# Kernel tuning notes

Measured on AMD Instinct MI355X. Metric: run time of the kernel, lower is better.

Reference implementation:

```python
import jax, jax.numpy as jnp
import numpy as np
from jax import lax

# module constants (from init_kwargs)
IN_CH = 128
OUT_CH = 128
CTX = 128
KS = 3
STRIDE = 1
PAD = 1
GROUPS = 1
ATT_GROUPS = 1
K = 4
TEMP = 30.0  # T_max, used as the fixed temperature at init


def setup_inputs() -> dict:
    key = jax.random.key(0)
    k1, k2, k3, k4, k5 = jax.random.split(key, 5)
    b, f, t = 16, 64, 256
    x = jax.random.normal(k1, (b, IN_CH, f, t), dtype=jnp.float32)
    g = jax.random.normal(k2, (1, b, CTX), dtype=jnp.float32)
    # Dense(k*att_groups) params (kaiming-normal kernel, zero bias)
    fan_in = CTX
    dense_kernel = jax.random.normal(k3, (CTX, K * ATT_GROUPS), dtype=jnp.float32) * np.sqrt(2.0 / fan_in)
    dense_bias = jnp.zeros((K * ATT_GROUPS,), dtype=jnp.float32)
    # kernel bank: (k, out, in//groups, ks, ks) -> swapaxes(1,2) -> flatten to (1, att_groups, k, -1)
    flat = OUT_CH * (IN_CH // GROUPS) * KS * KS // ATT_GROUPS
    weight = jax.random.normal(k4, (1, ATT_GROUPS, K, flat), dtype=jnp.float32) * np.sqrt(2.0 / flat)
    return {"x": x, "g": g, "dense_kernel": dense_kernel, "dense_bias": dense_bias, "weight": weight}


def reference(x, g, dense_kernel, dense_bias, weight):
    b, c, f, t = x.shape
    g_c = g[0].reshape(b, -1)                                  # [b, ctx]
    residuals = (g_c @ dense_kernel + dense_bias).reshape(b, ATT_GROUPS, 1, -1)  # [b, ag, 1, k]
    attention = jax.nn.softmax(residuals / TEMP, axis=-1)      # [b, ag, 1, k]
    # per-sample kernel aggregation: [b, ag, 1, k] @ [1, ag, k, D] -> [b, ag, 1, D]
    agg = (attention @ weight).swapaxes(1, 2)                  # [b, 1, ag, D]
    agg = agg.reshape(b * OUT_CH, IN_CH // GROUPS, KS, KS)
    # batch-as-groups grouped conv
    out = lax.conv_general_dilated(
        x.reshape(1, b * c, f, t), agg,
        window_strides=(STRIDE, STRIDE),
        padding=[(PAD, PAD), (PAD, PAD)],
        dimension_numbers=("NCHW", "OIHW", "NCHW"),
        feature_group_count=b * GROUPS,
    )
    return out.reshape(b, OUT_CH, out.shape[-2], out.shape[-1])
```

## Files before the change

### kernel.cpp

```cpp
#include <hip/hip_runtime.h>
#include <stdint.h>

#define NB 16
#define NC 128
#define NOC 128
#define NF 64
#define NT 256
#define NCTX 128
#define NTAPS 9
#define NFLAT 147456
#define TEMPR 30.0f

#define SXCOLS 130
#define SX_CHUNKS (4*SXCOLS)
#define SW_CHUNKS (3*4*NOC)

typedef float f32x4 __attribute__((ext_vector_type(4)));
typedef __bf16 bf16x8 __attribute__((ext_vector_type(8)));

__global__ void attn_kernel(const float* __restrict__ g,
                            const float* __restrict__ dk,
                            const float* __restrict__ bias,
                            float* __restrict__ att) {
    int b = threadIdx.x;
    if (b >= NB) return;
    float r0 = bias[0], r1 = bias[1], r2 = bias[2], r3 = bias[3];
    const float* gb = g + b * NCTX;
    for (int c = 0; c < NCTX; ++c) {
        float gv = gb[c];
        r0 += gv * dk[c*4+0];
        r1 += gv * dk[c*4+1];
        r2 += gv * dk[c*4+2];
        r3 += gv * dk[c*4+3];
    }
    r0 *= (1.0f/TEMPR); r1 *= (1.0f/TEMPR); r2 *= (1.0f/TEMPR); r3 *= (1.0f/TEMPR);
    float mx = fmaxf(fmaxf(r0, r1), fmaxf(r2, r3));
    float e0 = expf(r0-mx), e1 = expf(r1-mx), e2 = expf(r2-mx), e3 = expf(r3-mx);
    float s = e0+e1+e2+e3;
    att[b*4+0] = e0/s; att[b*4+1] = e1/s; att[b*4+2] = e2/s; att[b*4+3] = e3/s;
}

__global__ void agg_kernel(const float* __restrict__ w,
                           const float* __restrict__ att,
                           unsigned short* __restrict__ wb) {
    int idx = blockIdx.x * 256 + threadIdx.x;
    int ic = idx & 127;
    int oc = (idx >> 7) & 127;
    int b  = idx >> 14;
    float a0 = att[b*4+0], a1 = att[b*4+1], a2 = att[b*4+2], a3 = att[b*4+3];
    int d0 = (oc*NC + ic) * NTAPS;
    int c4 = ic >> 5;
    int kq = (ic >> 3) & 3;
    int e  = ic & 7;
    #pragma unroll
    for (int tap = 0; tap < NTAPS; ++tap) {
        float s = a0 * w[0*NFLAT + d0 + tap]
                + a1 * w[1*NFLAT + d0 + tap]
                + a2 * w[2*NFLAT + d0 + tap]
                + a3 * w[3*NFLAT + d0 + tap];
        __bf16 h = (__bf16)s;
        unsigned short u = *(unsigned short*)&h;
        int chunk = (tap * 4 + kq) * 128 + oc;
        wb[(((b * 4 + c4) * (NTAPS*4*NOC)) + chunk) * 8 + e] = u;
    }
}

__global__ __launch_bounds__(256) void conv_kernel(
        const float* __restrict__ x,
        const unsigned short* __restrict__ wb,
        float* __restrict__ out) {
    __shared__ __align__(16) unsigned short sx[SX_CHUNKS * 8];
    __shared__ __align__(16) unsigned short sw[SW_CHUNKS * 8];

    const int p  = blockIdx.x;
    const int lg = (p & 7) * 256 + (p >> 3);
    const int b  = lg >> 7;
    const int y  = (lg >> 1) & 63;
    const int t0 = (lg & 1) * 128;

    const int tid  = threadIdx.x;
    const int lane = tid & 63;
    const int wid  = tid >> 6;
    const int wpix = wid & 1;
    const int woc  = wid >> 1;
    const int l15  = lane & 15;
    const int l4   = lane >> 4;

    f32x4 acc[4][4];
    #pragma unroll
    for (int m = 0; m < 4; ++m)
        #pragma unroll
        for (int n = 0; n < 4; ++n)
            acc[m][n] = (f32x4){0.f, 0.f, 0.f, 0.f};

    const float* xb = x + (b * NC) * (NF * NT);
    const unsigned short* wbb = wb + b * (NTAPS * NOC * NC);

    const int se  = tid & 3;
    const int skq = (tid >> 2) & 3;

    const unsigned short* const swA = sw + ((l4 * NOC) + woc * 64 + l15) * 8;
    const unsigned short* const sxp = sx + (l4 * SXCOLS + wpix * 64 + l15) * 8;

    for (int c4 = 0; c4 < 4; ++c4) {
        #pragma unroll
        for (int ky = 0; ky < 3; ++ky) {
            const int iy = y - 1 + ky;
            const bool rowok = (unsigned)iy < (unsigned)NF;
            __syncthreads();

            #pragma unroll
            for (int j = 0; j < 2; ++j) {
                int u  = tid + j * 256;
                int q  = u >> 4;
                int ic = c4 * 32 + skq * 8 + se * 2;
                f32x4 v0 = (f32x4){0.f,0.f,0.f,0.f};
                f32x4 v1 = v0;
                if (rowok) {
                    const float* src = xb + (ic * NF + iy) * NT + t0 + q * 4;
                    v0 = *(const f32x4*)src;
                    v1 = *(const f32x4*)(src + NF * NT);
                }
                unsigned short* dst = sx + (skq * SXCOLS + q * 4 + 1) * 8 + se * 2;
                #pragma unroll
                for (int jj = 0; jj < 4; ++jj) {
                    __bf16 h0 = (__bf16)v0[jj];
                    __bf16 h1 = (__bf16)v1[jj];
                    unsigned pk = (unsigned)*(unsigned short*)&h0
                                | ((unsigned)*(unsigned short*)&h1 << 16);
                    *(unsigned*)(dst + jj * 8) = pk;
                }
            }
            if (tid < 32) {
                int e    = tid & 3;
                int kq   = (tid >> 2) & 3;
                int side = tid >> 4;
                int c    = side ? (SXCOLS - 1) : 0;
                int t    = t0 - 1 + c;
                int ic   = c4 * 32 + kq * 8 + e * 2;
                float f0 = 0.f, f1 = 0.f;
                if (rowok && (unsigned)t < (unsigned)NT) {
                    const float* src = xb + (ic * NF + iy) * NT + t;
                    f0 = src[0];
                    f1 = src[NF * NT];
                }
                __bf16 h0 = (__bf16)f0;
                __bf16 h1 = (__bf16)f1;
                unsigned pk = (unsigned)*(unsigned short*)&h0
                            | ((unsigned)*(unsigned short*)&h1 << 16);
                *(unsigned*)(sx + (kq * SXCOLS + c) * 8 + e * 2) = pk;
            }

            {
                const unsigned short* wsrc = wbb + ((c4 * 9 + ky * 3) * 4 * NOC) * 8;
                #pragma unroll
                for (int j = 0; j < 6; ++j) {
                    const int chunk = j * 256 + wid * 64;
                    __builtin_amdgcn_global_load_lds(
                        (const __attribute__((address_space(1))) unsigned int*)
                            (const void*)(wsrc + (chunk + lane) * 8),
                        (__attribute__((address_space(3))) unsigned int*)
                            (void*)(sw + chunk * 8),
                        16, 0, 0);
                }
            }
            __syncthreads();

            #pragma unroll
            for (int kx = 0; kx < 3; ++kx) {
                bf16x8 af[4], bfv[4];
                #pragma unroll
                for (int m = 0; m < 4; ++m)
                    af[m] = *(const bf16x8*)(swA + (kx * 4 * NOC + m * 16) * 8);
                #pragma unroll
                for (int n = 0; n < 4; ++n)
                    bfv[n] = *(const bf16x8*)(sxp + (kx + n * 16) * 8);
                #pragma unroll
                for (int m = 0; m < 4; ++m)
                    #pragma unroll
                    for (int n = 0; n < 4; ++n)
                        acc[m][n] = __builtin_amdgcn_mfma_f32_16x16x32_bf16(
                            af[m], bfv[n], acc[m][n], 0, 0, 0);
            }
        }
    }

    #pragma unroll
    for (int m = 0; m < 4; ++m) {
        int ocb = woc * 64 + m * 16 + l4 * 4;
        #pragma unroll
        for (int r = 0; r < 4; ++r) {
            float* orow = out + ((b * NOC + ocb + r) * NF + y) * NT + t0;
            #pragma unroll
            for (int n = 0; n < 4; ++n)
                orow[wpix * 64 + n * 16 + l15] = acc[m][n][r];
        }
    }
}

extern "C" void kernel_launch(void* const* d_in, const int* in_sizes, int n_in,
                              void* d_out, int out_size, void* d_ws, size_t ws_size,
                              hipStream_t stream) {
    const float* x    = (const float*)d_in[0];
    const float* g    = (const float*)d_in[1];
    const float* dk   = (const float*)d_in[2];
    const float* bias = (const float*)d_in[3];
    const float* w    = (const float*)d_in[4];
    float* out = (float*)d_out;

    float* att = (float*)d_ws;
    unsigned short* wb = (unsigned short*)((char*)d_ws + 256);

    attn_kernel<<<dim3(1), dim3(64), 0, stream>>>(g, dk, bias, att);
    agg_kernel<<<dim3(1024), dim3(256), 0, stream>>>(w, att, wb);
    conv_kernel<<<dim3(2048), dim3(256), 0, stream>>>(x, wb, out);
}
```

Before: 142.7 us.

## Double-buffer LDS tiles to prefetch next phase during MFMA compute

```diff
diff --git a/kernel.cpp b/kernel.cpp
--- a/kernel.cpp
+++ b/kernel.cpp
@@ -11,9 +11,9 @@
 #define NFLAT 147456
 #define TEMPR 30.0f
 
-#define SXCOLS 130
-#define SX_CHUNKS (4*SXCOLS)
-#define SW_CHUNKS (3*4*NOC)
+#define SW_CH 1536
+#define SX_CH 520
+#define BUF_CH (SW_CH + SX_CH)
 
 typedef float f32x4 __attribute__((ext_vector_type(4)));
 typedef __bf16 bf16x8 __attribute__((ext_vector_type(8)));
@@ -69,14 +69,13 @@
         const float* __restrict__ x,
         const unsigned short* __restrict__ wb,
         float* __restrict__ out) {
-    __shared__ __align__(16) unsigned short sx[SX_CHUNKS * 8];
-    __shared__ __align__(16) unsigned short sw[SW_CHUNKS * 8];
-
-    const int p  = blockIdx.x;
-    const int lg = (p & 7) * 256 + (p >> 3);
-    const int b  = lg >> 7;
-    const int y  = (lg >> 1) & 63;
-    const int t0 = (lg & 1) * 128;
+    __shared__ __align__(16) unsigned short lds[2 * BUF_CH * 8];
+
+    const int p_  = blockIdx.x;
+    const int lg  = (p_ & 7) * 256 + (p_ >> 3);
+    const int b   = lg >> 7;
+    const int y   = (lg >> 1) & 63;
+    const int t0  = (lg & 1) * 128;
 
     const int tid  = threadIdx.x;
     const int lane = tid & 63;
@@ -96,92 +95,132 @@
     const float* xb = x + (b * NC) * (NF * NT);
     const unsigned short* wbb = wb + b * (NTAPS * NOC * NC);
 
+    const int sq  = tid >> 4;
+    const int skq = (tid >> 2) & 3;
     const int se  = tid & 3;
-    const int skq = (tid >> 2) & 3;
-
-    const unsigned short* const swA = sw + ((l4 * NOC) + woc * 64 + l15) * 8;
-    const unsigned short* const sxp = sx + (l4 * SXCOLS + wpix * 64 + l15) * 8;
-
+
+    f32x4 v00, v01, v10, v11;
+    float bf0 = 0.f, bf1 = 0.f;
+
+    auto issue_x = [&](int c4, int ky) {
+        const int iy = y - 1 + ky;
+        const bool rowok = (unsigned)iy < (unsigned)NF;
+        const int ic0 = c4 * 32 + skq * 8 + se * 2;
+        v00 = (f32x4){0.f,0.f,0.f,0.f}; v01 = v00; v10 = v00; v11 = v00;
+        if (rowok) {
+            const float* src = xb + (ic0 * NF + iy) * NT + t0 + sq * 8;
+            v00 = *(const f32x4*)src;
+            v01 = *(const f32x4*)(src + 4);
+            v10 = *(const f32x4*)(src + NF * NT);
+            v11 = *(const f32x4*)(src + NF * NT + 4);
+        }
+        bf0 = 0.f; bf1 = 0.f;
+        if (tid < 32) {
+            const int side = (tid >> 4) & 1;
+            const int c    = side ? 129 : 0;
+            const int t    = t0 + c - 1;
+            const int ic   = c4 * 32 + skq * 8 + se * 2;
+            if (rowok && (unsigned)t < (unsigned)NT) {
+                const float* src = xb + (ic * NF + iy) * NT + t;
+                bf0 = src[0];
+                bf1 = src[NF * NT];
+            }
+        }
+    };
+
+    auto issue_w = [&](int c4, int ky, unsigned short* swb) {
+        const unsigned short* slice = wbb + (c4 * 4608 + ky * 1536) * 8;
+        #pragma unroll
+        for (int j = 0; j < 6; ++j) {
+            const int rid = j * 4 + wid;
+            __builtin_amdgcn_global_load_lds(
+                (const __attribute__((address_space(1))) unsigned int*)
+                    (const void*)(slice + (rid * 64 + lane) * 8),
+                (__attribute__((address_space(3))) unsigned int*)
+                    (void*)(swb + rid * 64 * 8),
+                16, 0, 0);
+        }
+    };
+
+    auto write_x = [&](unsigned short* sxb) {
+        unsigned short* dst = sxb + (skq * 130 + sq * 8 + 1) * 8 + se * 2;
+        #pragma unroll
+        for (int jj = 0; jj < 4; ++jj) {
+            __bf16 h0 = (__bf16)v00[jj];
+            __bf16 h1 = (__bf16)v10[jj];
+            unsigned pk = (unsigned)*(unsigned short*)&h0
+                        | ((unsigned)*(unsigned short*)&h1 << 16);
+            *(unsigned*)(dst + jj * 8) = pk;
+        }
+        #pragma unroll
+        for (int jj = 0; jj < 4; ++jj) {
+            __bf16 h0 = (__bf16)v01[jj];
+            __bf16 h1 = (__bf16)v11[jj];
+            unsigned pk = (unsigned)*(unsigned short*)&h0
+                        | ((unsigned)*(unsigned short*)&h1 << 16);
+            *(unsigned*)(dst + (4 + jj) * 8) = pk;
+        }
+        if (tid < 32) {
+            const int side = (tid >> 4) & 1;
+            const int c    = side ? 129 : 0;
+            __bf16 h0 = (__bf16)bf0;
+            __bf16 h1 = (__bf16)bf1;
+            unsigned pk = (unsigned)*(unsigned short*)&h0
+                        | ((unsigned)*(unsigned short*)&h1 << 16);
+            *(unsigned*)(sxb + (skq * 130 + c) * 8 + se * 2) = pk;
+        }
+    };
+
+    issue_x(0, 0);
+    issue_w(0, 0, lds);
+    asm volatile("s_waitcnt vmcnt(0)" ::: "memory");
+    write_x(lds + SW_CH * 8);
+    __syncthreads();
+
+    #pragma unroll
     for (int c4 = 0; c4 < 4; ++c4) {
         #pragma unroll
         for (int ky = 0; ky < 3; ++ky) {
-            const int iy = y - 1 + ky;
-            const bool rowok = (unsigned)iy < (unsigned)NF;
-            __syncthreads();
-
-            #pragma unroll
-            for (int j = 0; j < 2; ++j) {
-                int u  = tid + j * 256;
-                int q  = u >> 4;
-                int ic = c4 * 32 + skq * 8 + se * 2;
-                f32x4 v0 = (f32x4){0.f,0.f,0.f,0.f};
-                f32x4 v1 = v0;
-                if (rowok) {
-                    const float* src = xb + (ic * NF + iy) * NT + t0 + q * 4;
-                    v0 = *(const f32x4*)src;
-                    v1 = *(const f32x4*)(src + NF * NT);
-                }
-                unsigned short* dst = sx + (skq * SXCOLS + q * 4 + 1) * 8 + se * 2;
-                #pragma unroll
-                for (int jj = 0; jj < 4; ++jj) {
-                    __bf16 h0 = (__bf16)v0[jj];
-                    __bf16 h1 = (__bf16)v1[jj];
-                    unsigned pk = (unsigned)*(unsigned short*)&h0
-                                | ((unsigned)*(unsigned short*)&h1 << 16);
-                    *(unsigned*)(dst + jj * 8) = pk;
-                }
-            }
-            if (tid < 32) {
-                int e    = tid & 3;
-                int kq   = (tid >> 2) & 3;
-                int side = tid >> 4;
-                int c    = side ? (SXCOLS - 1) : 0;
-                int t    = t0 - 1 + c;
-                int ic   = c4 * 32 + kq * 8 + e * 2;
-                float f0 = 0.f, f1 = 0.f;
-                if (rowok && (unsigned)t < (unsigned)NT) {
-                    const float* src = xb + (ic * NF + iy) * NT + t;
-                    f0 = src[0];
-                    f1 = src[NF * NT];
-                }
-                __bf16 h0 = (__bf16)f0;
-                __bf16 h1 = (__bf16)f1;
-                unsigned pk = (unsigned)*(unsigned short*)&h0
-                            | ((unsigned)*(unsigned short*)&h1 << 16);
-                *(unsigned*)(sx + (kq * SXCOLS + c) * 8 + e * 2) = pk;
-            }
-
-            {
-                const unsigned short* wsrc = wbb + ((c4 * 9 + ky * 3) * 4 * NOC) * 8;
-                #pragma unroll
-                for (int j = 0; j < 6; ++j) {
-                    const int chunk = j * 256 + wid * 64;
-                    __builtin_amdgcn_global_load_lds(
-                        (const __attribute__((address_space(1))) unsigned int*)
-                            (const void*)(wsrc + (chunk + lane) * 8),
-                        (__attribute__((address_space(3))) unsigned int*)
-                            (void*)(sw + chunk * 8),
-                        16, 0, 0);
-                }
-            }
-            __syncthreads();
+            const int ph   = c4 * 3 + ky;
+            const int last = (ph == 11);
+            unsigned short* cur = lds + (ph & 1) * (BUF_CH * 8);
+            unsigned short* nxt = lds + ((ph & 1) ^ 1) * (BUF_CH * 8);
+            unsigned short* swb = cur;
+            unsigned short* sxb = cur + SW_CH * 8;
+
+            if (!last) {
+                const int nc4 = (ph + 1) / 3;
+                const int nky = (ph + 1) % 3;
+                issue_x(nc4, nky);
+                issue_w(nc4, nky, nxt);
+            }
 
             #pragma unroll
             for (int kx = 0; kx < 3; ++kx) {
                 bf16x8 af[4], bfv[4];
                 #pragma unroll
                 for (int m = 0; m < 4; ++m)
-                    af[m] = *(const bf16x8*)(swA + (kx * 4 * NOC + m * 16) * 8);
+                    af[m] = *(const bf16x8*)(swb +
+                        ((kx * 4 + l4) * 128 + woc * 64 + m * 16 + l15) * 8);
                 #pragma unroll
                 for (int n = 0; n < 4; ++n)
-                    bfv[n] = *(const bf16x8*)(sxp + (kx + n * 16) * 8);
+                    bfv[n] = *(const bf16x8*)(sxb +
+                        (l4 * 130 + wpix * 64 + n * 16 + l15 + kx) * 8);
+                __builtin_amdgcn_s_setprio(1);
                 #pragma unroll
                 for (int m = 0; m < 4; ++m)
                     #pragma unroll
                     for (int n = 0; n < 4; ++n)
                         acc[m][n] = __builtin_amdgcn_mfma_f32_16x16x32_bf16(
                             af[m], bfv[n], acc[m][n], 0, 0, 0);
-            }
+                __builtin_amdgcn_s_setprio(0);
+            }
+
+            if (!last) {
+                asm volatile("s_waitcnt vmcnt(0)" ::: "memory");
+                write_x(nxt + SW_CH * 8);
+            }
+            __syncthreads();
         }
     }
 
```

New measurement: 124.8 us. 1.14x faster.

## Load weight fragments directly from global into registers and stage all three input rows per channel chunk

Applied to the files above, without the earlier changes.

```diff
diff --git a/kernel.cpp b/kernel.cpp
--- a/kernel.cpp
+++ b/kernel.cpp
@@ -12,8 +12,7 @@
 #define TEMPR 30.0f
 
 #define SXCOLS 130
-#define SX_CHUNKS (4*SXCOLS)
-#define SW_CHUNKS (3*4*NOC)
+#define SX_CH (3*4*SXCOLS)
 
 typedef float f32x4 __attribute__((ext_vector_type(4)));
 typedef __bf16 bf16x8 __attribute__((ext_vector_type(8)));
@@ -69,14 +68,13 @@
         const float* __restrict__ x,
         const unsigned short* __restrict__ wb,
         float* __restrict__ out) {
-    __shared__ __align__(16) unsigned short sx[SX_CHUNKS * 8];
-    __shared__ __align__(16) unsigned short sw[SW_CHUNKS * 8];
-
-    const int p  = blockIdx.x;
-    const int lg = (p & 7) * 256 + (p >> 3);
-    const int b  = lg >> 7;
-    const int y  = (lg >> 1) & 63;
-    const int t0 = (lg & 1) * 128;
+    __shared__ __align__(16) unsigned short sx[SX_CH * 8];
+
+    const int p_  = blockIdx.x;
+    const int lg  = (p_ & 7) * 256 + (p_ >> 3);
+    const int b   = lg >> 7;
+    const int y   = (lg >> 1) & 63;
+    const int t0  = (lg & 1) * 128;
 
     const int tid  = threadIdx.x;
     const int lane = tid & 63;
@@ -94,94 +92,96 @@
             acc[m][n] = (f32x4){0.f, 0.f, 0.f, 0.f};
 
     const float* xb = x + (b * NC) * (NF * NT);
-    const unsigned short* wbb = wb + b * (NTAPS * NOC * NC);
-
-    const int se  = tid & 3;
-    const int skq = (tid >> 2) & 3;
-
-    const unsigned short* const swA = sw + ((l4 * NOC) + woc * 64 + l15) * 8;
+    const unsigned short* wbb = wb + b * (4 * NTAPS * 4 * NOC) * 8;
+
+    const unsigned short* const wfrag = wbb + (l4 * 128 + woc * 64 + l15) * 8;
+
     const unsigned short* const sxp = sx + (l4 * SXCOLS + wpix * 64 + l15) * 8;
 
     for (int c4 = 0; c4 < 4; ++c4) {
-        #pragma unroll
-        for (int ky = 0; ky < 3; ++ky) {
-            const int iy = y - 1 + ky;
-            const bool rowok = (unsigned)iy < (unsigned)NF;
-            __syncthreads();
-
-            #pragma unroll
-            for (int j = 0; j < 2; ++j) {
-                int u  = tid + j * 256;
-                int q  = u >> 4;
-                int ic = c4 * 32 + skq * 8 + se * 2;
-                f32x4 v0 = (f32x4){0.f,0.f,0.f,0.f};
-                f32x4 v1 = v0;
-                if (rowok) {
-                    const float* src = xb + (ic * NF + iy) * NT + t0 + q * 4;
-                    v0 = *(const f32x4*)src;
-                    v1 = *(const f32x4*)(src + NF * NT);
-                }
-                unsigned short* dst = sx + (skq * SXCOLS + q * 4 + 1) * 8 + se * 2;
-                #pragma unroll
-                for (int jj = 0; jj < 4; ++jj) {
-                    __bf16 h0 = (__bf16)v0[jj];
-                    __bf16 h1 = (__bf16)v1[jj];
-                    unsigned pk = (unsigned)*(unsigned short*)&h0
-                                | ((unsigned)*(unsigned short*)&h1 << 16);
-                    *(unsigned*)(dst + jj * 8) = pk;
-                }
-            }
-            if (tid < 32) {
-                int e    = tid & 3;
-                int kq   = (tid >> 2) & 3;
-                int side = tid >> 4;
-                int c    = side ? (SXCOLS - 1) : 0;
-                int t    = t0 - 1 + c;
-                int ic   = c4 * 32 + kq * 8 + e * 2;
-                float f0 = 0.f, f1 = 0.f;
-                if (rowok && (unsigned)t < (unsigned)NT) {
-                    const float* src = xb + (ic * NF + iy) * NT + t;
-                    f0 = src[0];
-                    f1 = src[NF * NT];
-                }
-                __bf16 h0 = (__bf16)f0;
-                __bf16 h1 = (__bf16)f1;
+        const int ic0 = c4 * 32;
+        const unsigned short* const wc4 = wfrag + (c4 * NTAPS * 4 * NOC) * 8;
+
+        bf16x8 afc0 = *(const bf16x8*)(wc4 + (0 * 16) * 8);
+        bf16x8 afc1 = *(const bf16x8*)(wc4 + (1 * 16) * 8);
+        bf16x8 afc2 = *(const bf16x8*)(wc4 + (2 * 16) * 8);
+        bf16x8 afc3 = *(const bf16x8*)(wc4 + (3 * 16) * 8);
+
+        __syncthreads();
+
+        #pragma unroll
+        for (int j = 0; j < 6; ++j) {
+            const int u  = tid + j * 256;
+            const int e  = u & 3;
+            const int kq = (u >> 2) & 3;
+            const int q  = (u >> 4) & 31;
+            const int r  = u >> 9;
+            const int iy = y - 1 + r;
+            const int ic = ic0 + kq * 8 + e * 2;
+            f32x4 v0 = (f32x4){0.f,0.f,0.f,0.f};
+            f32x4 v1 = v0;
+            if ((unsigned)iy < (unsigned)NF) {
+                const float* src = xb + (ic * NF + iy) * NT + t0 + q * 4;
+                v0 = *(const f32x4*)src;
+                v1 = *(const f32x4*)(src + NF * NT);
+            }
+            unsigned short* dst = sx + ((r * 4 + kq) * SXCOLS + q * 4 + 1) * 8 + e * 2;
+            #pragma unroll
+            for (int jj = 0; jj < 4; ++jj) {
+                __bf16 h0 = (__bf16)v0[jj];
+                __bf16 h1 = (__bf16)v1[jj];
                 unsigned pk = (unsigned)*(unsigned short*)&h0
                             | ((unsigned)*(unsigned short*)&h1 << 16);
-                *(unsigned*)(sx + (kq * SXCOLS + c) * 8 + e * 2) = pk;
-            }
-
-            {
-                const unsigned short* wsrc = wbb + ((c4 * 9 + ky * 3) * 4 * NOC) * 8;
-                #pragma unroll
-                for (int j = 0; j < 6; ++j) {
-                    const int chunk = j * 256 + wid * 64;
-                    __builtin_amdgcn_global_load_lds(
-                        (const __attribute__((address_space(1))) unsigned int*)
-                            (const void*)(wsrc + (chunk + lane) * 8),
-                        (__attribute__((address_space(3))) unsigned int*)
-                            (void*)(sw + chunk * 8),
-                        16, 0, 0);
-                }
-            }
-            __syncthreads();
-
-            #pragma unroll
-            for (int kx = 0; kx < 3; ++kx) {
-                bf16x8 af[4], bfv[4];
-                #pragma unroll
-                for (int m = 0; m < 4; ++m)
-                    af[m] = *(const bf16x8*)(swA + (kx * 4 * NOC + m * 16) * 8);
-                #pragma unroll
-                for (int n = 0; n < 4; ++n)
-                    bfv[n] = *(const bf16x8*)(sxp + (kx + n * 16) * 8);
-                #pragma unroll
-                for (int m = 0; m < 4; ++m)
-                    #pragma unroll
-                    for (int n = 0; n < 4; ++n)
-                        acc[m][n] = __builtin_amdgcn_mfma_f32_16x16x32_bf16(
-                            af[m], bfv[n], acc[m][n], 0, 0, 0);
-            }
+                *(unsigned*)(dst + jj * 8) = pk;
+            }
+        }
+        if (tid < 96) {
+            const int e    = tid & 3;
+            const int kq   = (tid >> 2) & 3;
+            const int side = (tid >> 4) & 1;
+            const int r    = tid >> 5;
+            const int c    = side ? (SXCOLS - 1) : 0;
+            const int t    = t0 - 1 + c;
+            const int iy   = y - 1 + r;
+            const int ic   = ic0 + kq * 8 + e * 2;
+            float f0 = 0.f, f1 = 0.f;
+            if ((unsigned)iy < (unsigned)NF && (unsigned)t < (unsigned)NT) {
+                const float* src = xb + (ic * NF + iy) * NT + t;
+                f0 = src[0];
+                f1 = src[NF * NT];
+            }
+            __bf16 h0 = (__bf16)f0;
+            __bf16 h1 = (__bf16)f1;
+            unsigned pk = (unsigned)*(unsigned short*)&h0
+                        | ((unsigned)*(unsigned short*)&h1 << 16);
+            *(unsigned*)(sx + ((r * 4 + kq) * SXCOLS + c) * 8 + e * 2) = pk;
+        }
+        __syncthreads();
+
+        #pragma unroll
+        for (int tap = 0; tap < 9; ++tap) {
+            const int ky = tap / 3;
+            const int kx = tap % 3;
+            bf16x8 afn0, afn1, afn2, afn3;
+            if (tap < 8) {
+                const unsigned short* wt = wc4 + ((tap + 1) * 4 * NOC) * 8;
+                afn0 = *(const bf16x8*)(wt + (0 * 16) * 8);
+                afn1 = *(const bf16x8*)(wt + (1 * 16) * 8);
+                afn2 = *(const bf16x8*)(wt + (2 * 16) * 8);
+                afn3 = *(const bf16x8*)(wt + (3 * 16) * 8);
+            }
+            bf16x8 bfv[4];
+            #pragma unroll
+            for (int n = 0; n < 4; ++n)
+                bfv[n] = *(const bf16x8*)(sxp + (ky * 4 * SXCOLS + n * 16 + kx) * 8);
+            #pragma unroll
+            for (int n = 0; n < 4; ++n) {
+                acc[0][n] = __builtin_amdgcn_mfma_f32_16x16x32_bf16(afc0, bfv[n], acc[0][n], 0, 0, 0);
+                acc[1][n] = __builtin_amdgcn_mfma_f32_16x16x32_bf16(afc1, bfv[n], acc[1][n], 0, 0, 0);
+                acc[2][n] = __builtin_amdgcn_mfma_f32_16x16x32_bf16(afc2, bfv[n], acc[2][n], 0, 0, 0);
+                acc[3][n] = __builtin_amdgcn_mfma_f32_16x16x32_bf16(afc3, bfv[n], acc[3][n], 0, 0, 0);
+            }
+            if (tap < 8) { afc0 = afn0; afc1 = afn1; afc2 = afn2; afc3 = afn3; }
         }
     }
 
```

Result: faster. 129.4 us (-9.3%).
